# Kernel optimization log

Hardware: AMD Instinct MI355X
Metric: run time of the kernel (lower is better)

Reference implementation:

```python
import jax, jax.numpy as jnp
import numpy as np

NUM_LAYERS = 3
INPUT_SIZE = 32
NUM_CAT = 64
EMB = 64
NQ = 1            # num_queries
B = 16
N = 2048
DIN = INPUT_SIZE + NUM_CAT + EMB  # 160, columns of W_e_proj


def setup_inputs() -> dict:
    key = jax.random.key(0)
    k1, k2, k3, k4 = jax.random.split(key, 4)
    return {
        "x": jax.random.normal(k1, (B, DIN, N), dtype=jnp.float32),
        "alpha": jax.random.normal(k2, (NUM_LAYERS, EMB), dtype=jnp.float32),
        "kernel_param": jnp.ones((1,), dtype=jnp.float32),
        "embedding_matrix": jax.random.normal(k3, (EMB, NUM_CAT), dtype=jnp.float32),
        "M": jax.random.normal(k4, (EMB, EMB), dtype=jnp.float32),
    }


def reference(x, alpha, kernel_param, embedding_matrix, M):
    # Input projection h = W_e_proj @ x. W_e_proj is block-structured:
    #   rows [0,is)        : identity on x[:is]
    #   rows [is, is+emb)  : embedding_matrix @ x[is:is+num_cat]
    #   rows [-emb:]       : identity on x[-emb:]
    h = jnp.concatenate([
        x[:, :INPUT_SIZE],
        jnp.einsum('ec,bcn->ben', embedding_matrix,
                   x[:, INPUT_SIZE:INPUT_SIZE + NUM_CAT]),
        x[:, -EMB:],
    ], axis=1)  # [B, INPUT_SIZE + 2*EMB, N]

    kp = kernel_param[0]
    for nl in range(NUM_LAYERS):
        kv = h[:, :, :-NQ]          # keys/values exclude the query tokens
        n_ctx = kv.shape[-1]
        # W_Q, W_K are identity on the first INPUT_SIZE rows, zero elsewhere
        xq = h[:, :INPUT_SIZE]      # [B, is, N]
        xk = kv[:, :INPUT_SIZE]     # [B, is, Nk]
        # linear kernel scores
        scores = kp * jnp.einsum('bim,bin->bmn', xq, xk)   # [B, N, Nk]
        # W_V is zero except diag(alpha[nl]) on the middle EMB block
        v_mid = alpha[nl][:, None] * kv[:, INPUT_SIZE:INPUT_SIZE + EMB]  # [B, EMB, Nk]
        attn_mid = jnp.einsum('bin,bmn->bim', v_mid, scores) / n_ctx     # [B, EMB, N]
        # Output projection P^T: middle rows get M @ attn_mid,
        # bottom EMB rows get attn_mid (identity), first rows zero.
        upd = jnp.concatenate([
            jnp.zeros((h.shape[0], INPUT_SIZE, h.shape[2]), h.dtype),
            jnp.einsum('ji,bim->bjm', M, attn_mid),
            attn_mid,
        ], axis=1)
        h = h + upd

    f = h[:, -EMB:, :]                                    # [B, EMB, N]
    logits = jnp.einsum('bdn,dc->bnc', f, embedding_matrix)  # [B, N, C]
    predictions = jax.nn.softmax(logits, axis=-1)
    return logits, predictions
```

## Files before the change

### kernel.cpp

```cpp
#include <hip/hip_runtime.h>

#define BB 16
#define NN 2048
#define DIN 160
#define IS 32
#define NCAT 64
#define EMBD 64
#define NCTX 2047
#define SS 66
#define NTILE 32
#define GRID1 (BB * NTILE)
#define NPART (NTILE * 4)

__global__ __launch_bounds__(256) void k_gram(
    const float* __restrict__ x,
    float* __restrict__ Pg, float* __restrict__ Pk)
{
    __shared__ float xs[96 * SS];
    const int t = threadIdx.x;
    const int blk = blockIdx.x;
    const int b = blk >> 5;
    const int tile = blk & 31;
    const int n0 = tile << 6;
    const float* xb = x + (size_t)b * DIN * NN;

    for (int idx = t; idx < 96 * 32; idx += 256) {
        const int r = idx >> 5;
        const int mc = (idx & 31) << 1;
        float2 v = *(const float2*)&xb[r * NN + n0 + mc];
        if (n0 + mc + 1 == NCTX) v.y = 0.f;
        *(float2*)&xs[r * SS + mc] = v;
    }
    __syncthreads();

    const int mg = t >> 6;
    const int lane = t & 63;
    const int i4 = lane >> 3;
    const int d4 = lane & 7;
    const int i0 = i4 << 2;
    const int d0 = d4 << 2;
    const int m0 = mg << 4;

    float g[4][4], kk[8][4];
#pragma unroll
    for (int ii = 0; ii < 4; ii++)
#pragma unroll
        for (int jj = 0; jj < 4; jj++) g[ii][jj] = 0.f;
#pragma unroll
    for (int ii = 0; ii < 8; ii++)
#pragma unroll
        for (int jj = 0; jj < 4; jj++) kk[ii][jj] = 0.f;

    for (int m = m0; m < m0 + 16; m += 2) {
        float2 q[4], a[4], c[8];
#pragma unroll
        for (int j = 0; j < 4; j++) q[j] = *(const float2*)&xs[(d0 + j) * SS + m];
#pragma unroll
        for (int j = 0; j < 4; j++) a[j] = *(const float2*)&xs[(i0 + j) * SS + m];
#pragma unroll
        for (int j = 0; j < 8; j++) c[j] = *(const float2*)&xs[(32 + i4 + 8 * j) * SS + m];
#pragma unroll
        for (int ii = 0; ii < 4; ii++)
#pragma unroll
            for (int jj = 0; jj < 4; jj++)
                g[ii][jj] += a[ii].x * q[jj].x + a[ii].y * q[jj].y;
#pragma unroll
        for (int ii = 0; ii < 8; ii++)
#pragma unroll
            for (int jj = 0; jj < 4; jj++)
                kk[ii][jj] += c[ii].x * q[jj].x + c[ii].y * q[jj].y;
    }

    const size_t slot = (size_t)blk * 4 + mg;
    float* pg = Pg + slot * 1024;
#pragma unroll
    for (int ii = 0; ii < 4; ii++)
        *(float4*)&pg[(i0 + ii) * 32 + d0] = *(float4*)&g[ii][0];
    float* pk = Pk + slot * 2048;
#pragma unroll
    for (int ii = 0; ii < 8; ii++)
        *(float4*)&pk[(i4 + 8 * ii) * 32 + d0] = *(float4*)&kk[ii][0];
}

__global__ __launch_bounds__(256) void k_chain(const float* __restrict__ Pg,
                                               const float* __restrict__ Pk,
                                               const float* __restrict__ alpha,
                                               const float* __restrict__ kp,
                                               const float* __restrict__ emb,
                                               const float* __restrict__ Mm,
                                               float* __restrict__ Ubuf) {
    __shared__ float G_s[32][36];
    __shared__ float K_s[64][36];
    __shared__ float C_s[64][36];
    __shared__ float W_s[64][36];
    __shared__ float T_s[64][36];
    const int t = threadIdx.x;
    const int b = blockIdx.x;

    {
        const int row = t >> 3, col = (t & 7) << 2;
        float4 s = {0, 0, 0, 0};
        const float* base = Pg + (size_t)b * NPART * 1024 + row * 32 + col;
#pragma unroll 8
        for (int p = 0; p < NPART; p++) {
            float4 v = *(const float4*)(base + (size_t)p * 1024);
            s.x += v.x; s.y += v.y; s.z += v.z; s.w += v.w;
        }
        *(float4*)&G_s[row][col] = s;
    }
    {
        const int row0 = t >> 2, col = (t & 3) << 3;
        const float* base = Pk + (size_t)b * NPART * 2048 + row0 * 32 + col;
        float4 s0 = {0, 0, 0, 0}, s1 = {0, 0, 0, 0};
#pragma unroll 8
        for (int p = 0; p < NPART; p++) {
            float4 v0 = *(const float4*)(base + (size_t)p * 2048);
            float4 v1 = *(const float4*)(base + (size_t)p * 2048 + 4);
            s0.x += v0.x; s0.y += v0.y; s0.z += v0.z; s0.w += v0.w;
            s1.x += v1.x; s1.y += v1.y; s1.z += v1.z; s1.w += v1.w;
        }
        *(float4*)&K_s[row0][col] = s0;
        *(float4*)&K_s[row0][col + 4] = s1;
    }
    __syncthreads();

    const int r  = t >> 2;
    const int dd = (t & 3) << 3;

    {
        const float* er = emb + r * EMBD;
        float acc[8];
#pragma unroll
        for (int j = 0; j < 8; j++) acc[j] = 0.f;
        for (int c = 0; c < 64; c++) {
            const float e = er[c];
#pragma unroll
            for (int j = 0; j < 8; j++) acc[j] += e * K_s[c][dd + j];
        }
#pragma unroll
        for (int j = 0; j < 8; j++) C_s[r][dd + j] = acc[j];
    }
    __syncthreads();

    const float scale = kp[0] * (1.f / (float)NCTX);
    for (int l = 0; l < 3; l++) {
        const float f = scale * alpha[l * EMBD + r];
#pragma unroll
        for (int j = 0; j < 8; j++) {
            const float w = f * C_s[r][dd + j];
            if (l == 0) W_s[r][dd + j] = w; else W_s[r][dd + j] += w;
        }
        if (l < 2) {
            float tacc[8];
#pragma unroll
            for (int j = 0; j < 8; j++) tacc[j] = 0.f;
            for (int d = 0; d < 32; d++) {
                const float cv = C_s[r][d];
#pragma unroll
                for (int j = 0; j < 8; j++) tacc[j] += cv * G_s[d][dd + j];
            }
#pragma unroll
            for (int j = 0; j < 8; j++) T_s[r][dd + j] = f * tacc[j];
            __syncthreads();
            const float* Mr = Mm + r * EMBD;
            float uacc[8];
#pragma unroll
            for (int j = 0; j < 8; j++) uacc[j] = 0.f;
            for (int jj = 0; jj < 64; jj++) {
                const float mv = Mr[jj];
#pragma unroll
                for (int j = 0; j < 8; j++) uacc[j] += mv * T_s[jj][dd + j];
            }
#pragma unroll
            for (int j = 0; j < 8; j++) C_s[r][dd + j] += uacc[j];
            __syncthreads();
        }
    }
    __syncthreads();

    {
        float acc[8];
#pragma unroll
        for (int j = 0; j < 8; j++) acc[j] = 0.f;
        for (int e = 0; e < 64; e++) {
            const float ev = emb[e * EMBD + r];
#pragma unroll
            for (int j = 0; j < 8; j++) acc[j] += ev * W_s[e][dd + j];
        }
        float* Ur = Ubuf + (size_t)b * 2048 + r * 32 + dd;
#pragma unroll
        for (int j = 0; j < 8; j++) Ur[j] = acc[j];
    }
}

__global__ __launch_bounds__(256) void k_out(const float* __restrict__ x,
                                             const float* __restrict__ emb,
                                             const float* __restrict__ Ubuf,
                                             float* __restrict__ out) {
    __shared__ float lg_s[128][68];
    const int t = threadIdx.x;
    const int blk = blockIdx.x;
    const int b = blk >> 4;
    const int tile = blk & 15;
    const int h = t >> 7;
    const int nl = t & 127;
    const int n = (tile << 7) + nl;
    const int c0 = h << 5;
    const float* xb = x + (size_t)b * DIN * NN;

    float xq[IS];
#pragma unroll
    for (int d = 0; d < IS; d++) xq[d] = xb[d * NN + n];

    float lg[32];
    const float* Ub = Ubuf + (size_t)b * 2048;
#pragma unroll 4
    for (int cl = 0; cl < 32; cl++) {
        const float* Ur = Ub + (c0 + cl) * 32;
        float s = 0.f;
#pragma unroll
        for (int k = 0; k < 8; k++) {
            float4 u = *(const float4*)&Ur[4 * k];
            s += u.x * xq[4*k] + u.y * xq[4*k+1] + u.z * xq[4*k+2] + u.w * xq[4*k+3];
        }
        lg[cl] = s;
    }
    for (int e = 0; e < 64; e++) {
        const float tv = xb[(IS + NCAT + e) * NN + n];
        const float* er = emb + e * EMBD + c0;
#pragma unroll
        for (int cl = 0; cl < 32; cl++) lg[cl] += er[cl] * tv;
    }

    const size_t base = ((size_t)b * NN + n) * (size_t)NCAT;
    float* lo = out + base + c0;
#pragma unroll
    for (int k = 0; k < 8; k++) {
        float4 v = {lg[4*k], lg[4*k+1], lg[4*k+2], lg[4*k+3]};
        *(float4*)&lo[4*k] = v;
        *(float4*)&lg_s[nl][c0 + 4*k] = v;
    }
    __syncthreads();

    const int o0 = (1 - h) << 5;
    float mx = lg[0];
#pragma unroll
    for (int cl = 1; cl < 32; cl++) mx = fmaxf(mx, lg[cl]);
    float og[32];
#pragma unroll
    for (int k = 0; k < 8; k++) {
        float4 v = *(const float4*)&lg_s[nl][o0 + 4*k];
        og[4*k] = v.x; og[4*k+1] = v.y; og[4*k+2] = v.z; og[4*k+3] = v.w;
    }
#pragma unroll
    for (int cl = 0; cl < 32; cl++) mx = fmaxf(mx, og[cl]);

    float sum = 0.f;
#pragma unroll
    for (int cl = 0; cl < 32; cl++) {
        lg[cl] = __expf(lg[cl] - mx);
        sum += lg[cl];
    }
#pragma unroll
    for (int cl = 0; cl < 32; cl++) sum += __expf(og[cl] - mx);

    const float inv = 1.f / sum;
    float* po = out + (size_t)BB * NN * NCAT + base + c0;
#pragma unroll
    for (int k = 0; k < 8; k++) {
        float4 v = {lg[4*k]*inv, lg[4*k+1]*inv, lg[4*k+2]*inv, lg[4*k+3]*inv};
        *(float4*)&po[4*k] = v;
    }
}

extern "C" void kernel_launch(void* const* d_in, const int* in_sizes, int n_in,
                              void* d_out, int out_size, void* d_ws, size_t ws_size,
                              hipStream_t stream) {
    const float* x     = (const float*)d_in[0];
    const float* alpha = (const float*)d_in[1];
    const float* kp    = (const float*)d_in[2];
    const float* emb   = (const float*)d_in[3];
    const float* Mmat  = (const float*)d_in[4];
    float* out = (float*)d_out;

    float* Pg   = (float*)d_ws;
    float* Pk   = Pg + (size_t)GRID1 * 4 * 1024;
    float* Ubuf = Pk + (size_t)GRID1 * 4 * 2048;

    k_gram <<<GRID1, 256, 0, stream>>>(x, Pg, Pk);
    k_chain<<<BB,    256, 0, stream>>>(Pg, Pk, alpha, kp, emb, Mmat, Ubuf);
    k_out  <<<256,   256, 0, stream>>>(x, emb, Ubuf, out);
}
```

Baseline: 147.3 us.

## Reduce gram partials in-block and fuse chain into output kernel

Inside k_gram, the four warp-group partial Gram/K sums are now reduced through shared memory, so each block writes one partial instead of four. This cuts partial-buffer traffic and the reduction length in the consumer by 4x. The small per-batch chain kernel is fused into k_out: every output block recomputes its batch's 64x32 U matrix in shared memory, which removes a launch and the Ubuf round trip. The cost is that the chain work, including reading 32 partials, is repeated 16 times per batch, and the larger shared-memory footprint may reduce occupancy.

```diff
diff --git a/kernel.cpp b/kernel.cpp
--- a/kernel.cpp
+++ b/kernel.cpp
@@ -10,13 +10,14 @@
 #define SS 66
 #define NTILE 32
 #define GRID1 (BB * NTILE)
-#define NPART (NTILE * 4)
+#define NPART NTILE
 
 __global__ __launch_bounds__(256) void k_gram(
     const float* __restrict__ x,
     float* __restrict__ Pg, float* __restrict__ Pk)
 {
     __shared__ float xs[96 * SS];
+    __shared__ float cbuf[3 * 64 * 52];
     const int t = threadIdx.x;
     const int blk = blockIdx.x;
     const int b = blk >> 5;
@@ -71,31 +72,57 @@
                 kk[ii][jj] += c[ii].x * q[jj].x + c[ii].y * q[jj].y;
     }
 
-    const size_t slot = (size_t)blk * 4 + mg;
-    float* pg = Pg + slot * 1024;
-#pragma unroll
-    for (int ii = 0; ii < 4; ii++)
-        *(float4*)&pg[(i0 + ii) * 32 + d0] = *(float4*)&g[ii][0];
-    float* pk = Pk + slot * 2048;
-#pragma unroll
-    for (int ii = 0; ii < 8; ii++)
-        *(float4*)&pk[(i4 + 8 * ii) * 32 + d0] = *(float4*)&kk[ii][0];
+    if (mg > 0) {
+        float* p = cbuf + ((mg - 1) * 64 + lane) * 52;
+#pragma unroll
+        for (int ii = 0; ii < 4; ii++) *(float4*)&p[ii * 4] = *(float4*)&g[ii][0];
+#pragma unroll
+        for (int ii = 0; ii < 8; ii++) *(float4*)&p[16 + ii * 4] = *(float4*)&kk[ii][0];
+    }
+    __syncthreads();
+    if (mg == 0) {
+#pragma unroll
+        for (int w = 0; w < 3; w++) {
+            const float* p = cbuf + (w * 64 + lane) * 52;
+#pragma unroll
+            for (int ii = 0; ii < 4; ii++) {
+                float4 v = *(const float4*)&p[ii * 4];
+                g[ii][0] += v.x; g[ii][1] += v.y; g[ii][2] += v.z; g[ii][3] += v.w;
+            }
+#pragma unroll
+            for (int ii = 0; ii < 8; ii++) {
+                float4 v = *(const float4*)&p[16 + ii * 4];
+                kk[ii][0] += v.x; kk[ii][1] += v.y; kk[ii][2] += v.z; kk[ii][3] += v.w;
+            }
+        }
+        float* pg = Pg + (size_t)blk * 1024;
+#pragma unroll
+        for (int ii = 0; ii < 4; ii++)
+            *(float4*)&pg[(i0 + ii) * 32 + d0] = *(float4*)&g[ii][0];
+        float* pk = Pk + (size_t)blk * 2048;
+#pragma unroll
+        for (int ii = 0; ii < 8; ii++)
+            *(float4*)&pk[(i4 + 8 * ii) * 32 + d0] = *(float4*)&kk[ii][0];
+    }
 }
 
-__global__ __launch_bounds__(256) void k_chain(const float* __restrict__ Pg,
-                                               const float* __restrict__ Pk,
-                                               const float* __restrict__ alpha,
-                                               const float* __restrict__ kp,
-                                               const float* __restrict__ emb,
-                                               const float* __restrict__ Mm,
-                                               float* __restrict__ Ubuf) {
+__global__ __launch_bounds__(256) void k_out(
+    const float* __restrict__ x, const float* __restrict__ Pg,
+    const float* __restrict__ Pk, const float* __restrict__ alpha,
+    const float* __restrict__ kp, const float* __restrict__ emb,
+    const float* __restrict__ Mm, float* __restrict__ out)
+{
     __shared__ float G_s[32][36];
     __shared__ float K_s[64][36];
     __shared__ float C_s[64][36];
     __shared__ float W_s[64][36];
-    __shared__ float T_s[64][36];
+    __shared__ float U_s[64][36];
+    __shared__ float lg_s[128][68];
     const int t = threadIdx.x;
-    const int b = blockIdx.x;
+    const int blk = blockIdx.x;
+    const int b = blk >> 4;
+    const int tile = blk & 15;
+    const float* xb = x + (size_t)b * DIN * NN;
 
     {
         const int row = t >> 3, col = (t & 7) << 2;
@@ -126,7 +153,6 @@
 
     const int r  = t >> 2;
     const int dd = (t & 3) << 3;
-
     {
         const float* er = emb + r * EMBD;
         float acc[8];
@@ -160,7 +186,7 @@
                 for (int j = 0; j < 8; j++) tacc[j] += cv * G_s[d][dd + j];
             }
 #pragma unroll
-            for (int j = 0; j < 8; j++) T_s[r][dd + j] = f * tacc[j];
+            for (int j = 0; j < 8; j++) U_s[r][dd + j] = f * tacc[j];
             __syncthreads();
             const float* Mr = Mm + r * EMBD;
             float uacc[8];
@@ -169,7 +195,7 @@
             for (int jj = 0; jj < 64; jj++) {
                 const float mv = Mr[jj];
 #pragma unroll
-                for (int j = 0; j < 8; j++) uacc[j] += mv * T_s[jj][dd + j];
+                for (int j = 0; j < 8; j++) uacc[j] += mv * U_s[jj][dd + j];
             }
 #pragma unroll
             for (int j = 0; j < 8; j++) C_s[r][dd + j] += uacc[j];
@@ -187,36 +213,24 @@
 #pragma unroll
             for (int j = 0; j < 8; j++) acc[j] += ev * W_s[e][dd + j];
         }
-        float* Ur = Ubuf + (size_t)b * 2048 + r * 32 + dd;
-#pragma unroll
-        for (int j = 0; j < 8; j++) Ur[j] = acc[j];
-    }
-}
-
-__global__ __launch_bounds__(256) void k_out(const float* __restrict__ x,
-                                             const float* __restrict__ emb,
-                                             const float* __restrict__ Ubuf,
-                                             float* __restrict__ out) {
-    __shared__ float lg_s[128][68];
-    const int t = threadIdx.x;
-    const int blk = blockIdx.x;
-    const int b = blk >> 4;
-    const int tile = blk & 15;
+#pragma unroll
+        for (int j = 0; j < 8; j++) U_s[r][dd + j] = acc[j];
+    }
+    __syncthreads();
+
     const int h = t >> 7;
     const int nl = t & 127;
     const int n = (tile << 7) + nl;
     const int c0 = h << 5;
-    const float* xb = x + (size_t)b * DIN * NN;
 
     float xq[IS];
 #pragma unroll
     for (int d = 0; d < IS; d++) xq[d] = xb[d * NN + n];
 
     float lg[32];
-    const float* Ub = Ubuf + (size_t)b * 2048;
 #pragma unroll 4
     for (int cl = 0; cl < 32; cl++) {
-        const float* Ur = Ub + (c0 + cl) * 32;
+        const float* Ur = &U_s[c0 + cl][0];
         float s = 0.f;
 #pragma unroll
         for (int k = 0; k < 8; k++) {
@@ -283,11 +297,9 @@
     const float* Mmat  = (const float*)d_in[4];
     float* out = (float*)d_out;
 
-    float* Pg   = (float*)d_ws;
-    float* Pk   = Pg + (size_t)GRID1 * 4 * 1024;
-    float* Ubuf = Pk + (size_t)GRID1 * 4 * 2048;
-
-    k_gram <<<GRID1, 256, 0, stream>>>(x, Pg, Pk);
-    k_chain<<<BB,    256, 0, stream>>>(Pg, Pk, alpha, kp, emb, Mmat, Ubuf);
-    k_out  <<<256,   256, 0, stream>>>(x, emb, Ubuf, out);
+    float* Pg = (float*)d_ws;
+    float* Pk = Pg + (size_t)GRID1 * 1024;
+
+    k_gram<<<GRID1, 256, 0, stream>>>(x, Pg, Pk);
+    k_out <<<256,   256, 0, stream>>>(x, Pg, Pk, alpha, kp, emb, Mmat, out);
 }
```

Result: faster. 125.9 us (-14.5%).

## Reduce gram partials in shared memory and split softmax output across four warps

Applied to the files above, without the earlier changes.

k_gram now sums the four per-wave partial Gram/K tiles in LDS before writing, so it emits one partial per block instead of four. This shrinks workspace writes and the reads k_chain must do. k_out now gives each thread 16 classes instead of 32 and doubles the grid to 512 blocks. It combines the softmax across the four class slices with a max/sum merge done through small shared arrays. The trade is more blocks, duplicated xq loads and extra exps, in exchange for lower register pressure and better occupancy.

```diff
diff --git a/kernel.cpp b/kernel.cpp
--- a/kernel.cpp
+++ b/kernel.cpp
@@ -10,13 +10,14 @@
 #define SS 66
 #define NTILE 32
 #define GRID1 (BB * NTILE)
-#define NPART (NTILE * 4)
+#define NPART NTILE
 
 __global__ __launch_bounds__(256) void k_gram(
     const float* __restrict__ x,
     float* __restrict__ Pg, float* __restrict__ Pk)
 {
     __shared__ float xs[96 * SS];
+    __shared__ float cbuf[3 * 64 * 52];
     const int t = threadIdx.x;
     const int blk = blockIdx.x;
     const int b = blk >> 5;
@@ -71,15 +72,38 @@
                 kk[ii][jj] += c[ii].x * q[jj].x + c[ii].y * q[jj].y;
     }
 
-    const size_t slot = (size_t)blk * 4 + mg;
-    float* pg = Pg + slot * 1024;
-#pragma unroll
-    for (int ii = 0; ii < 4; ii++)
-        *(float4*)&pg[(i0 + ii) * 32 + d0] = *(float4*)&g[ii][0];
-    float* pk = Pk + slot * 2048;
-#pragma unroll
-    for (int ii = 0; ii < 8; ii++)
-        *(float4*)&pk[(i4 + 8 * ii) * 32 + d0] = *(float4*)&kk[ii][0];
+    if (mg > 0) {
+        float* p = cbuf + ((mg - 1) * 64 + lane) * 52;
+#pragma unroll
+        for (int ii = 0; ii < 4; ii++) *(float4*)&p[ii * 4] = *(float4*)&g[ii][0];
+#pragma unroll
+        for (int ii = 0; ii < 8; ii++) *(float4*)&p[16 + ii * 4] = *(float4*)&kk[ii][0];
+    }
+    __syncthreads();
+    if (mg == 0) {
+#pragma unroll
+        for (int w = 0; w < 3; w++) {
+            const float* p = cbuf + (w * 64 + lane) * 52;
+#pragma unroll
+            for (int ii = 0; ii < 4; ii++) {
+                float4 v = *(const float4*)&p[ii * 4];
+                g[ii][0] += v.x; g[ii][1] += v.y; g[ii][2] += v.z; g[ii][3] += v.w;
+            }
+#pragma unroll
+            for (int ii = 0; ii < 8; ii++) {
+                float4 v = *(const float4*)&p[16 + ii * 4];
+                kk[ii][0] += v.x; kk[ii][1] += v.y; kk[ii][2] += v.z; kk[ii][3] += v.w;
+            }
+        }
+        float* pg = Pg + (size_t)blk * 1024;
+#pragma unroll
+        for (int ii = 0; ii < 4; ii++)
+            *(float4*)&pg[(i0 + ii) * 32 + d0] = *(float4*)&g[ii][0];
+        float* pk = Pk + (size_t)blk * 2048;
+#pragma unroll
+        for (int ii = 0; ii < 8; ii++)
+            *(float4*)&pk[(i4 + 8 * ii) * 32 + d0] = *(float4*)&kk[ii][0];
+    }
 }
 
 __global__ __launch_bounds__(256) void k_chain(const float* __restrict__ Pg,
@@ -194,29 +218,30 @@
 }
 
 __global__ __launch_bounds__(256) void k_out(const float* __restrict__ x,
+                                             const float* __restrict__ Ubuf,
                                              const float* __restrict__ emb,
-                                             const float* __restrict__ Ubuf,
                                              float* __restrict__ out) {
-    __shared__ float lg_s[128][68];
+    __shared__ float pm_s[4][68];
+    __shared__ float ps_s[4][68];
     const int t = threadIdx.x;
+    const int q = t >> 6;
+    const int nl = t & 63;
     const int blk = blockIdx.x;
-    const int b = blk >> 4;
-    const int tile = blk & 15;
-    const int h = t >> 7;
-    const int nl = t & 127;
-    const int n = (tile << 7) + nl;
-    const int c0 = h << 5;
+    const int b = blk >> 5;
+    const int tile = blk & 31;
+    const int n = (tile << 6) + nl;
+    const int c0 = q << 4;
     const float* xb = x + (size_t)b * DIN * NN;
 
     float xq[IS];
 #pragma unroll
     for (int d = 0; d < IS; d++) xq[d] = xb[d * NN + n];
 
-    float lg[32];
-    const float* Ub = Ubuf + (size_t)b * 2048;
-#pragma unroll 4
-    for (int cl = 0; cl < 32; cl++) {
-        const float* Ur = Ub + (c0 + cl) * 32;
+    float lg[16];
+    const float* Ub = Ubuf + (size_t)b * 2048 + c0 * 32;
+#pragma unroll
+    for (int cl = 0; cl < 16; cl++) {
+        const float* Ur = Ub + cl * 32;
         float s = 0.f;
 #pragma unroll
         for (int k = 0; k < 8; k++) {
@@ -225,50 +250,48 @@
         }
         lg[cl] = s;
     }
+
+#pragma unroll 4
     for (int e = 0; e < 64; e++) {
         const float tv = xb[(IS + NCAT + e) * NN + n];
         const float* er = emb + e * EMBD + c0;
 #pragma unroll
-        for (int cl = 0; cl < 32; cl++) lg[cl] += er[cl] * tv;
+        for (int cl = 0; cl < 16; cl++) lg[cl] += er[cl] * tv;
     }
 
     const size_t base = ((size_t)b * NN + n) * (size_t)NCAT;
     float* lo = out + base + c0;
 #pragma unroll
-    for (int k = 0; k < 8; k++) {
+    for (int k = 0; k < 4; k++) {
         float4 v = {lg[4*k], lg[4*k+1], lg[4*k+2], lg[4*k+3]};
         *(float4*)&lo[4*k] = v;
-        *(float4*)&lg_s[nl][c0 + 4*k] = v;
-    }
-    __syncthreads();
-
-    const int o0 = (1 - h) << 5;
-    float mx = lg[0];
-#pragma unroll
-    for (int cl = 1; cl < 32; cl++) mx = fmaxf(mx, lg[cl]);
-    float og[32];
-#pragma unroll
-    for (int k = 0; k < 8; k++) {
-        float4 v = *(const float4*)&lg_s[nl][o0 + 4*k];
-        og[4*k] = v.x; og[4*k+1] = v.y; og[4*k+2] = v.z; og[4*k+3] = v.w;
-    }
-#pragma unroll
-    for (int cl = 0; cl < 32; cl++) mx = fmaxf(mx, og[cl]);
-
-    float sum = 0.f;
-#pragma unroll
-    for (int cl = 0; cl < 32; cl++) {
-        lg[cl] = __expf(lg[cl] - mx);
-        sum += lg[cl];
-    }
-#pragma unroll
-    for (int cl = 0; cl < 32; cl++) sum += __expf(og[cl] - mx);
-
-    const float inv = 1.f / sum;
+    }
+
+    float pmax = lg[0];
+#pragma unroll
+    for (int cl = 1; cl < 16; cl++) pmax = fmaxf(pmax, lg[cl]);
+    float el[16];
+    float psum = 0.f;
+#pragma unroll
+    for (int cl = 0; cl < 16; cl++) {
+        el[cl] = __expf(lg[cl] - pmax);
+        psum += el[cl];
+    }
+    pm_s[q][nl] = pmax;
+    ps_s[q][nl] = psum;
+    __syncthreads();
+
+    float m0 = pm_s[0][nl], m1 = pm_s[1][nl], m2 = pm_s[2][nl], m3 = pm_s[3][nl];
+    float s0 = ps_s[0][nl], s1 = ps_s[1][nl], s2 = ps_s[2][nl], s3 = ps_s[3][nl];
+    float mx = fmaxf(fmaxf(m0, m1), fmaxf(m2, m3));
+    float sum = s0 * __expf(m0 - mx) + s1 * __expf(m1 - mx)
+              + s2 * __expf(m2 - mx) + s3 * __expf(m3 - mx);
+    const float f = __expf(pmax - mx) / sum;
+
     float* po = out + (size_t)BB * NN * NCAT + base + c0;
 #pragma unroll
-    for (int k = 0; k < 8; k++) {
-        float4 v = {lg[4*k]*inv, lg[4*k+1]*inv, lg[4*k+2]*inv, lg[4*k+3]*inv};
+    for (int k = 0; k < 4; k++) {
+        float4 v = {el[4*k] * f, el[4*k+1] * f, el[4*k+2] * f, el[4*k+3] * f};
         *(float4*)&po[4*k] = v;
     }
 }
@@ -284,10 +307,10 @@
     float* out = (float*)d_out;
 
     float* Pg   = (float*)d_ws;
-    float* Pk   = Pg + (size_t)GRID1 * 4 * 1024;
-    float* Ubuf = Pk + (size_t)GRID1 * 4 * 2048;
+    float* Pk   = Pg + (size_t)GRID1 * 1024;
+    float* Ubuf = Pk + (size_t)GRID1 * 2048;
 
     k_gram <<<GRID1, 256, 0, stream>>>(x, Pg, Pk);
     k_chain<<<BB,    256, 0, stream>>>(Pg, Pk, alpha, kp, emb, Mmat, Ubuf);
-    k_out  <<<256,   256, 0, stream>>>(x, emb, Ubuf, out);
+    k_out  <<<512,   256, 0, stream>>>(x, Ubuf, emb, out);
 }
```

Measured after the change: 132.0 us. -10.4%, faster.
